# Kernel optimization log

Hardware: AMD Instinct MI355X
Metric: run time of the kernel (lower is better)

Reference implementation:

```python
import jax, jax.numpy as jnp
import numpy as np

EMB_DIM = 1024
NUM_HEADS = 16
HEAD_DIM = EMB_DIM // NUM_HEADS  # 64
B, S = 2, 2048


def setup_inputs() -> dict:
    key = jax.random.key(0)
    ks = jax.random.split(key, 9)
    scale = 1.0 / np.sqrt(EMB_DIM)
    return {
        "query": jax.random.normal(ks[0], (B, S, EMB_DIM), dtype=jnp.float32),
        "Wq": jax.random.normal(ks[1], (EMB_DIM, EMB_DIM), dtype=jnp.float32) * scale,
        "bq": jax.random.normal(ks[2], (EMB_DIM,), dtype=jnp.float32) * 0.01,
        "Wk": jax.random.normal(ks[3], (EMB_DIM, EMB_DIM), dtype=jnp.float32) * scale,
        "bk": jax.random.normal(ks[4], (EMB_DIM,), dtype=jnp.float32) * 0.01,
        "Wv": jax.random.normal(ks[5], (EMB_DIM, EMB_DIM), dtype=jnp.float32) * scale,
        "bv": jax.random.normal(ks[6], (EMB_DIM,), dtype=jnp.float32) * 0.01,
        "Wo": jax.random.normal(ks[7], (EMB_DIM, EMB_DIM), dtype=jnp.float32) * scale,
        "bo": jax.random.normal(ks[8], (EMB_DIM,), dtype=jnp.float32) * 0.01,
    }


def reference(query, Wq, bq, Wk, bk, Wv, bv, Wo, bo):
    # Self-attention path (key_value=None, mask=None in the original forward).
    b, s, _ = query.shape
    # torch nn.Linear: y = x @ W.T + b
    def proj(x, W, bias):
        y = jnp.einsum('bse,fe->bsf', x, W) + bias
        # [B,S,E] -> [B,H,S,D]
        return y.reshape(b, s, NUM_HEADS, HEAD_DIM).transpose(0, 2, 1, 3)

    q = proj(query, Wq, bq)
    k = proj(query, Wk, bk)
    v = proj(query, Wv, bv)

    scores = jnp.einsum('bhqd,bhkd->bhqk', q, k) / np.sqrt(HEAD_DIM).astype(np.float32)
    attn = jax.nn.softmax(scores, axis=-1)  # [B,H,S,S]
    out = jnp.einsum('bhqk,bhkd->bhqd', attn, v)
    out = out.transpose(0, 2, 1, 3).reshape(b, s, EMB_DIM)
    return jnp.einsum('bse,fe->bsf', out, Wo) + bo
```

## Files before the change

### kernel.cpp

```cpp
#include <hip/hip_runtime.h>
#include <hip/hip_bf16.h>

using bf16x4 = __attribute__((ext_vector_type(4))) short;
using short8 = __attribute__((ext_vector_type(8))) short;
using f32x4  = __attribute__((ext_vector_type(4))) float;
using f32x16 = __attribute__((ext_vector_type(16))) float;
using u32x2  = __attribute__((ext_vector_type(2))) unsigned;

__device__ __forceinline__ short f2bf(float f) {
  unsigned u = __builtin_bit_cast(unsigned, f);
  u = (u + 0x7fffu + ((u >> 16) & 1u)) >> 16;
  return (short)u;
}
__device__ __forceinline__ unsigned pk2(float a, float b) {
  __hip_bfloat162 h = __float22bfloat162_rn(make_float2(a, b));
  unsigned u; __builtin_memcpy(&u, &h, 4);
  return u;
}
__device__ __forceinline__ void gload16(const short* g, short* l) {
  __builtin_amdgcn_global_load_lds(
      (const __attribute__((address_space(1))) unsigned int*)g,
      (__attribute__((address_space(3))) unsigned int*)l, 16, 0, 0);
}
__device__ __forceinline__ void pl32swap(unsigned &a, unsigned &b) {
  asm("v_permlane32_swap_b32 %0, %1" : "+v"(a), "+v"(b));
}

constexpr int E  = 1024;
constexpr int SL = 2048;
constexpr int NB = 2;
constexpr int NH = 16;
constexpr int M  = NB * SL;

__global__ __launch_bounds__(256) void convert_kernel(
    const float* __restrict__ X,  const float* __restrict__ Wq,
    const float* __restrict__ Wk, const float* __restrict__ Wv,
    const float* __restrict__ Wo, short* __restrict__ out)
{
  const size_t i8 = ((size_t)blockIdx.x * 256 + threadIdx.x) * 8;
  const float* src;
  if (i8 < (size_t)(4u << 20)) {
    src = X + i8;
  } else {
    size_t r = i8 - (size_t)(4u << 20);
    int wi = (int)(r >> 20);
    size_t off = r & ((1u << 20) - 1);
    src = (wi == 0 ? Wq : wi == 1 ? Wk : wi == 2 ? Wv : Wo) + off;
  }
  f32x4 a = *(const f32x4*)src;
  f32x4 b = *(const f32x4*)(src + 4);
  short hb[8];
#pragma unroll
  for (int e = 0; e < 4; ++e) { hb[e] = f2bf(a[e]); hb[4 + e] = f2bf(b[e]); }
  *(short8*)(out + i8) = *(short8*)hb;
}

template <bool OUTF32, bool PROJ>
__device__ __forceinline__ void gemm_body(
    const short* __restrict__ A0, const short* __restrict__ A1, const short* __restrict__ A2,
    const short* __restrict__ B0, const short* __restrict__ B1, const short* __restrict__ B2,
    const float* __restrict__ b0, const float* __restrict__ b1, const float* __restrict__ b2,
    void* __restrict__ Y0, void* __restrict__ Y1, void* __restrict__ Y2,
    float s0, float s1, float s2, int ld0, int ld1, int ld2)
{
  constexpr int BK = 32;
  constexpr int TM = 128, TN = 64;
  constexpr int RA = TM / 64;
  constexpr int RB = TN / 64;
  constexpr int WM = TM / 2, WN = TN / 2;
  constexpr int NI = WM / 16, NJ = WN / 16;
  __shared__ alignas(16) short As[2][TM * BK];
  __shared__ alignas(16) short Bs[2][TN * BK];
  const int t = threadIdx.x;
  const int l = t & 63;
  const int w = t >> 6;
  const int c = l & 15;
  const int g = l >> 4;
  const int z = blockIdx.z;
  const short* Ap = (z == 0) ? A0 : (z == 1) ? A1 : A2;
  const short* Bp = (z == 0) ? B0 : (z == 1) ? B1 : B2;
  const float* bp = (z == 0) ? b0 : (z == 1) ? b1 : b2;
  void* Yp        = (z == 0) ? Y0 : (z == 1) ? Y1 : Y2;
  const float sc  = (z == 0) ? s0 : (z == 1) ? s1 : s2;
  const int ldY   = (z == 0) ? ld0 : (z == 1) ? ld1 : ld2;
  const bool swp  = PROJ ? (z != 2) : true;
  int m0, n0;
  if (PROJ && z == 2) {
    const int idx = (int)blockIdx.y * 64 + (int)blockIdx.x;
    m0 = (idx & 31) * TM;
    n0 = (idx >> 5) * TN;
  } else {
    m0 = (int)blockIdx.y * TM;
    n0 = (int)blockIdx.x * TN;
  }

  const short* gA[RA]; int oA[RA];
  const short* gB[RB]; int oB[RB];
#pragma unroll
  for (int r = 0; r < RA; ++r) {
    const int cc = r * 256 + t;
    gA[r] = Ap + (size_t)(m0 + (cc >> 2)) * E + (cc & 3) * 8;
    oA[r] = (r * 256 + (t & ~63)) * 8;
  }
#pragma unroll
  for (int r = 0; r < RB; ++r) {
    const int cc = r * 256 + t;
    gB[r] = Bp + (size_t)(n0 + (cc >> 2)) * E + (cc & 3) * 8;
    oB[r] = (r * 256 + (t & ~63)) * 8;
  }

#pragma unroll
  for (int r = 0; r < RA; ++r) gload16(gA[r], &As[0][oA[r]]);
#pragma unroll
  for (int r = 0; r < RB; ++r) gload16(gB[r], &Bs[0][oB[r]]);

  const int wm = (w >> 1) * WM;
  const int wn = (w & 1) * WN;
  f32x4 acc[NI][NJ] = {};
  int cur = 0;

  for (int k0 = 0; k0 < E; k0 += BK) {
    __syncthreads();
    if (k0 + BK < E) {
#pragma unroll
      for (int r = 0; r < RA; ++r) gload16(gA[r] + k0 + BK, &As[cur ^ 1][oA[r]]);
#pragma unroll
      for (int r = 0; r < RB; ++r) gload16(gB[r] + k0 + BK, &Bs[cur ^ 1][oB[r]]);
    }
    short8 ah[NI], bfr[NJ];
#pragma unroll
    for (int i = 0; i < NI; ++i)
      ah[i] = *(const short8*)&As[cur][(wm + i * 16 + c) * BK + g * 8];
#pragma unroll
    for (int j = 0; j < NJ; ++j)
      bfr[j] = *(const short8*)&Bs[cur][(wn + j * 16 + c) * BK + g * 8];
#pragma unroll
    for (int i = 0; i < NI; ++i)
#pragma unroll
      for (int j = 0; j < NJ; ++j)
        acc[i][j] = __builtin_amdgcn_mfma_f32_16x16x32_bf16(ah[i], bfr[j], acc[i][j], 0, 0, 0);
    cur ^= 1;
  }

  float bm[NI][4];
  if (swp) {
#pragma unroll
    for (int i = 0; i < NI; ++i)
#pragma unroll
      for (int r = 0; r < 4; ++r)
        bm[i][r] = bp[m0 + wm + i * 16 + g * 4 + r];
  }
#pragma unroll
  for (int j = 0; j < NJ; ++j) {
    const int col = n0 + wn + j * 16 + c;
    const float bj = swp ? 0.f : bp[col];
#pragma unroll
    for (int i = 0; i < NI; ++i) {
      const int row = m0 + wm + i * 16 + g * 4;
      float v[4];
#pragma unroll
      for (int r = 0; r < 4; ++r)
        v[r] = (acc[i][j][r] + (swp ? bm[i][r] : bj)) * sc;
      if (OUTF32) {
        f32x4 o = {v[0], v[1], v[2], v[3]};
        *(f32x4*)((float*)Yp + (size_t)col * ldY + row) = o;
      } else {
        u32x2 o = {pk2(v[0], v[1]), pk2(v[2], v[3])};
        *(u32x2*)((short*)Yp + (size_t)col * ldY + row) = o;
      }
    }
  }
}

__global__ __launch_bounds__(256) void proj_kernel(
    const short* A0, const short* A1, const short* A2,
    const short* B0, const short* B1, const short* B2,
    const float* b0, const float* b1, const float* b2,
    void* Y0, void* Y1, void* Y2,
    float s0, float s1, float s2, int ld0, int ld1, int ld2)
{
  gemm_body<false, true>(A0, A1, A2, B0, B1, B2, b0, b1, b2,
                         Y0, Y1, Y2, s0, s1, s2, ld0, ld1, ld2);
}

__global__ __launch_bounds__(256) void out_kernel(
    const short* A0, const short* A1, const short* A2,
    const short* B0, const short* B1, const short* B2,
    const float* b0, const float* b1, const float* b2,
    void* Y0, void* Y1, void* Y2,
    float s0, float s1, float s2, int ld0, int ld1, int ld2)
{
  gemm_body<true, false>(A0, A1, A2, B0, B1, B2, b0, b1, b2,
                         Y0, Y1, Y2, s0, s1, s2, ld0, ld1, ld2);
}

__global__ __launch_bounds__(256, 2) void flash_kernel(
    const short* __restrict__ Qm, const short* __restrict__ Km,
    const short* __restrict__ VTm, short* __restrict__ Oh)
{
  __shared__ alignas(16) short Ks[2][64][64];
  __shared__ alignas(16) short Vt[2][64][64];
  const int t = threadIdx.x;
  const int l = t & 63;
  const int w = t >> 6;
  const int c = l & 31;
  const int hi = l >> 5;
  const int q0 = blockIdx.x * 128;
  const int bh = (int)blockIdx.y;
  const int bat = bh >> 4;
  const int h = bh & 15;
  const size_t baseK = (size_t)bat * SL * E + h * 64;
  const size_t baseV = (size_t)(h * 64) * M + (size_t)bat * SL;

  short8 qf[4];
  {
    const short* qp = Qm + baseK + (size_t)(q0 + w * 32 + c) * E + hi * 8;
#pragma unroll
    for (int tt = 0; tt < 4; ++tt) qf[tt] = *(const short8*)(qp + tt * 16);
  }

  const int sr = t >> 3, sg = t & 7;
  const int swz = (sg ^ (sr & 7)) * 8;
  const short* gK0 = Km + baseK + (size_t)sr * E + sg * 8;
  const short* gK1 = gK0 + (size_t)32 * E;
  const short* gV0 = VTm + baseV + (size_t)sr * M + sg * 8;
  const short* gV1 = gV0 + (size_t)32 * M;
  const int wo0 = sr * 64 + swz;
  const int wo1 = (sr + 32) * 64 + swz;

  short8 k0r, k1r, v0r, v1r;
  k0r = *(const short8*)gK0; k1r = *(const short8*)gK1;
  v0r = *(const short8*)gV0; v1r = *(const short8*)gV1;
  *(short8*)(&Ks[0][0][0] + wo0) = k0r; *(short8*)(&Ks[0][0][0] + wo1) = k1r;
  *(short8*)(&Vt[0][0][0] + wo0) = v0r; *(short8*)(&Vt[0][0][0] + wo1) = v1r;
  k0r = *(const short8*)(gK0 + (size_t)64 * E);
  k1r = *(const short8*)(gK1 + (size_t)64 * E);
  v0r = *(const short8*)(gV0 + 64);
  v1r = *(const short8*)(gV1 + 64);

  f32x16 oa0 = {}, oa1 = {};
  f32x4 lacc = {0.f, 0.f, 0.f, 0.f};
  __syncthreads();

  constexpr int NTT = SL / 64;
  const int sx = c & 7;
  for (int kt = 0; kt < NTT; ++kt) {
    const int cur = kt & 1;
    if (kt + 1 < NTT) {
      short* Kn = &Ks[cur ^ 1][0][0];
      short* Vn = &Vt[cur ^ 1][0][0];
      *(short8*)(Kn + wo0) = k0r; *(short8*)(Kn + wo1) = k1r;
      *(short8*)(Vn + wo0) = v0r; *(short8*)(Vn + wo1) = v1r;
      if (kt + 2 < NTT) {
        const size_t ko = (size_t)(kt + 2) * 64 * E;
        const int vo = (kt + 2) * 64;
        k0r = *(const short8*)(gK0 + ko); k1r = *(const short8*)(gK1 + ko);
        v0r = *(const short8*)(gV0 + vo); v1r = *(const short8*)(gV1 + vo);
      }
    }
    const short* Kc0 = &Ks[cur][c][0];
    const short* Kc1 = &Ks[cur][32 + c][0];
    const short* Vc0 = &Vt[cur][c][0];
    const short* Vc1 = &Vt[cur][32 + c][0];

    f32x16 st0 = {}, st1 = {};
    __builtin_amdgcn_s_setprio(1);
#pragma unroll
    for (int tt = 0; tt < 4; ++tt) {
      const int off = ((tt * 2 + hi) ^ sx) * 8;
      short8 kf0 = *(const short8*)(Kc0 + off);
      short8 kf1 = *(const short8*)(Kc1 + off);
      st0 = __builtin_amdgcn_mfma_f32_32x32x16_bf16(kf0, qf[tt], st0, 0, 0, 0);
      st1 = __builtin_amdgcn_mfma_f32_32x32x16_bf16(kf1, qf[tt], st1, 0, 0, 0);
    }
    __builtin_amdgcn_s_setprio(0);

    float p0[16], p1[16];
#pragma unroll
    for (int i = 0; i < 16; ++i) p0[i] = __builtin_amdgcn_exp2f(st0[i]);
#pragma unroll
    for (int i = 0; i < 16; ++i) p1[i] = __builtin_amdgcn_exp2f(st1[i]);
#pragma unroll
    for (int i = 0; i < 16; ++i) lacc[i & 3] += p0[i] + p1[i];

    unsigned W0[4][2], W1[4][2];
#pragma unroll
    for (int b8 = 0; b8 < 4; ++b8) {
      W0[b8][0] = pk2(p0[4 * b8 + 0], p0[4 * b8 + 1]);
      W0[b8][1] = pk2(p0[4 * b8 + 2], p0[4 * b8 + 3]);
      W1[b8][0] = pk2(p1[4 * b8 + 0], p1[4 * b8 + 1]);
      W1[b8][1] = pk2(p1[4 * b8 + 2], p1[4 * b8 + 3]);
    }

    __builtin_amdgcn_s_setprio(1);
#pragma unroll
    for (int tt = 0; tt < 4; ++tt) {
      unsigned a0, a1, b0, b1;
      if (tt == 0)      { a0 = W0[0][0]; a1 = W0[0][1]; b0 = W0[1][0]; b1 = W0[1][1]; }
      else if (tt == 1) { a0 = W0[2][0]; a1 = W0[2][1]; b0 = W0[3][0]; b1 = W0[3][1]; }
      else if (tt == 2) { a0 = W1[0][0]; a1 = W1[0][1]; b0 = W1[1][0]; b1 = W1[1][1]; }
      else              { a0 = W1[2][0]; a1 = W1[2][1]; b0 = W1[3][0]; b1 = W1[3][1]; }
      pl32swap(a0, b0);
      pl32swap(a1, b1);
      union { unsigned u[4]; short8 s8; } pf;
      pf.u[0] = a0; pf.u[1] = a1; pf.u[2] = b0; pf.u[3] = b1;
      const int off = ((tt * 2 + hi) ^ sx) * 8;
      short8 vf0 = *(const short8*)(Vc0 + off);
      short8 vf1 = *(const short8*)(Vc1 + off);
      oa0 = __builtin_amdgcn_mfma_f32_32x32x16_bf16(vf0, pf.s8, oa0, 0, 0, 0);
      oa1 = __builtin_amdgcn_mfma_f32_32x32x16_bf16(vf1, pf.s8, oa1, 0, 0, 0);
    }
    __builtin_amdgcn_s_setprio(0);
    __syncthreads();
  }

  float s = lacc[0] + lacc[1] + lacc[2] + lacc[3];
  s += __shfl_xor(s, 32);
  const float inv = 1.0f / s;
  const int q = q0 + w * 32 + c;
  short* op = Oh + ((size_t)bat * SL + q) * E + h * 64 + hi * 4;
#pragma unroll
  for (int b8 = 0; b8 < 4; ++b8) {
    u32x2 t0 = {pk2(oa0[4 * b8 + 0] * inv, oa0[4 * b8 + 1] * inv),
                pk2(oa0[4 * b8 + 2] * inv, oa0[4 * b8 + 3] * inv)};
    *(u32x2*)(op + b8 * 8) = t0;
    u32x2 t1 = {pk2(oa1[4 * b8 + 0] * inv, oa1[4 * b8 + 1] * inv),
                pk2(oa1[4 * b8 + 2] * inv, oa1[4 * b8 + 3] * inv)};
    *(u32x2*)(op + 32 + b8 * 8) = t1;
  }
}

extern "C" void kernel_launch(void* const* d_in, const int* in_sizes, int n_in,
                              void* d_out, int out_size, void* d_ws, size_t ws_size,
                              hipStream_t stream)
{
  const float* X  = (const float*)d_in[0];
  const float* Wq = (const float*)d_in[1];
  const float* bq = (const float*)d_in[2];
  const float* Wk = (const float*)d_in[3];
  const float* bk = (const float*)d_in[4];
  const float* Wv = (const float*)d_in[5];
  const float* bv = (const float*)d_in[6];
  const float* Wo = (const float*)d_in[7];
  const float* bo = (const float*)d_in[8];
  float* out = (float*)d_out;

  const size_t szX = (size_t)M * E;
  const size_t szW = (size_t)E * E;
  short* Xb  = (short*)d_ws;
  short* Wqb = Xb + szX;
  short* Wkb = Wqb + szW;
  short* Wvb = Wkb + szW;
  short* Wob = Wvb + szW;
  short* Qw  = Wob + szW;
  short* Kw  = Qw + szX;
  short* VTw = Kw + szX;

  convert_kernel<<<4096, 256, 0, stream>>>(X, Wq, Wk, Wv, Wo, Xb);

  const float kLog2eOver8 = 0.18033688011112042f;
  dim3 g1(M / 64, E / 128, 3);
  proj_kernel<<<g1, 256, 0, stream>>>(
      Wqb, Wkb, Xb,
      Xb, Xb, Wvb,
      bq, bk, bv,
      (void*)Qw, (void*)Kw, (void*)VTw,
      kLog2eOver8, 1.0f, 1.0f, E, E, M);

  dim3 g2(SL / 128, NB * NH);
  flash_kernel<<<g2, 256, 0, stream>>>(Qw, Kw, VTw, Qw );

  dim3 g3(M / 64, E / 128, 1);
  out_kernel<<<g3, 256, 0, stream>>>(
      Wob, Wob, Wob,
      Qw, Qw, Qw,
      bo, bo, bo,
      (void*)out, (void*)out, (void*)out,
      1.0f, 1.0f, 1.0f, E, E, E);
}
```

Measured before the change: 211.0 us.

## Enlarge GEMM N tile to 128 and remap blocks for XCD-aware locality

The GEMM tile grows from 128x64 to 128x128, halving the block count for the projection and output GEMMs. All three kernels now use a 1D grid whose block ids are remapped so that consecutive original tiles land on the same XCD (fid&7 chunking). This is meant to raise data reuse per block and improve L2 locality across the 8 XCDs. The trade-off is fewer blocks, which may lower occupancy, and more register and LDS use per block.

```diff
diff --git a/kernel.cpp b/kernel.cpp
--- a/kernel.cpp
+++ b/kernel.cpp
@@ -64,7 +64,7 @@
     float s0, float s1, float s2, int ld0, int ld1, int ld2)
 {
   constexpr int BK = 32;
-  constexpr int TM = 128, TN = 64;
+  constexpr int TM = 128, TN = 128;
   constexpr int RA = TM / 64;
   constexpr int RB = TN / 64;
   constexpr int WM = TM / 2, WN = TN / 2;
@@ -76,7 +76,22 @@
   const int w = t >> 6;
   const int c = l & 15;
   const int g = l >> 4;
-  const int z = blockIdx.z;
+
+  const int fid = (int)blockIdx.x;
+  int z, m0, n0;
+  if (PROJ) {
+    const int orig = (fid & 7) * 96 + (fid >> 3);
+    z = orig >> 8;
+    const int rem = orig & 255;
+    const bool sw = (z != 2);
+    m0 = (sw ? (rem >> 5) : (rem & 31)) * TM;
+    n0 = (sw ? (rem & 31) : (rem >> 5)) * TN;
+  } else {
+    const int orig = (fid & 7) * 32 + (fid >> 3);
+    z = 0;
+    m0 = (orig >> 5) * TM;
+    n0 = (orig & 31) * TN;
+  }
   const short* Ap = (z == 0) ? A0 : (z == 1) ? A1 : A2;
   const short* Bp = (z == 0) ? B0 : (z == 1) ? B1 : B2;
   const float* bp = (z == 0) ? b0 : (z == 1) ? b1 : b2;
@@ -84,15 +99,6 @@
   const float sc  = (z == 0) ? s0 : (z == 1) ? s1 : s2;
   const int ldY   = (z == 0) ? ld0 : (z == 1) ? ld1 : ld2;
   const bool swp  = PROJ ? (z != 2) : true;
-  int m0, n0;
-  if (PROJ && z == 2) {
-    const int idx = (int)blockIdx.y * 64 + (int)blockIdx.x;
-    m0 = (idx & 31) * TM;
-    n0 = (idx >> 5) * TN;
-  } else {
-    m0 = (int)blockIdx.y * TM;
-    n0 = (int)blockIdx.x * TN;
-  }
 
   const short* gA[RA]; int oA[RA];
   const short* gB[RB]; int oB[RB];
@@ -205,8 +211,10 @@
   const int w = t >> 6;
   const int c = l & 31;
   const int hi = l >> 5;
-  const int q0 = blockIdx.x * 128;
-  const int bh = (int)blockIdx.y;
+  const int fid = (int)blockIdx.x;
+  const int orig = (fid & 7) * 64 + (fid >> 3);
+  const int q0 = (orig & 15) * 128;
+  const int bh = orig >> 4;
   const int bat = bh >> 4;
   const int h = bh & 15;
   const size_t baseK = (size_t)bat * SL * E + h * 64;
@@ -359,19 +367,16 @@
   convert_kernel<<<4096, 256, 0, stream>>>(X, Wq, Wk, Wv, Wo, Xb);
 
   const float kLog2eOver8 = 0.18033688011112042f;
-  dim3 g1(M / 64, E / 128, 3);
-  proj_kernel<<<g1, 256, 0, stream>>>(
+  proj_kernel<<<768, 256, 0, stream>>>(
       Wqb, Wkb, Xb,
       Xb, Xb, Wvb,
       bq, bk, bv,
       (void*)Qw, (void*)Kw, (void*)VTw,
       kLog2eOver8, 1.0f, 1.0f, E, E, M);
 
-  dim3 g2(SL / 128, NB * NH);
-  flash_kernel<<<g2, 256, 0, stream>>>(Qw, Kw, VTw, Qw );
-
-  dim3 g3(M / 64, E / 128, 1);
-  out_kernel<<<g3, 256, 0, stream>>>(
+  flash_kernel<<<512, 256, 0, stream>>>(Qw, Kw, VTw, Qw );
+
+  out_kernel<<<256, 256, 0, stream>>>(
       Wob, Wob, Wob,
       Qw, Qw, Qw,
       bo, bo, bo,
```

Result: faster. 192.3 us (-8.9%).
